# Optimization experiments

Hardware: AMD Instinct MI355X
Metric: run time of the kernel (lower is better)

The kernel has to match this reference:

```python
import jax, jax.numpy as jnp
import numpy as np

N_NODES = 50000
N_EDGES = 800000
N_GRAPHS = 64
HEADS = 4
IN_CH, HID_CH, OUT_CH = 128, 64, 32


def setup_inputs() -> dict:
    key = jax.random.key(0)
    ks = jax.random.split(key, 13)
    x = jax.random.normal(ks[0], (N_NODES, IN_CH), dtype=jnp.float32)
    edge_index = jax.random.randint(ks[1], (2, N_EDGES), 0, N_NODES, dtype=jnp.int64)
    tensor_batch = jnp.sort(jax.random.randint(ks[2], (N_NODES,), 0, N_GRAPHS, dtype=jnp.int64))
    s = 0.1
    return {
        "x": x,
        "edge_index": edge_index,
        "tensor_batch": tensor_batch,
        "W1": jax.random.normal(ks[3], (IN_CH, HEADS * HID_CH), dtype=jnp.float32) * s,
        "a_src1": jax.random.normal(ks[4], (HEADS, HID_CH), dtype=jnp.float32) * s,
        "a_dst1": jax.random.normal(ks[5], (HEADS, HID_CH), dtype=jnp.float32) * s,
        "b1": jnp.zeros((HEADS * HID_CH,), dtype=jnp.float32),
        "W2": jax.random.normal(ks[6], (HEADS * HID_CH, HEADS * OUT_CH), dtype=jnp.float32) * s,
        "a_src2": jax.random.normal(ks[7], (HEADS, OUT_CH), dtype=jnp.float32) * s,
        "a_dst2": jax.random.normal(ks[8], (HEADS, OUT_CH), dtype=jnp.float32) * s,
        "b2": jnp.zeros((HEADS * OUT_CH,), dtype=jnp.float32),
        "Wout": jax.random.normal(ks[9], (HEADS * OUT_CH, 2), dtype=jnp.float32) * s,
        "bout": jnp.zeros((2,), dtype=jnp.float32),
    }


def gat_conv(x, src, dst, W, a_src, a_dst, b, heads, ch):
    """PyG-style GATConv (eval mode, self-loops already appended)."""
    N = x.shape[0]
    h = (x @ W).reshape(N, heads, ch)            # [N,H,C] per-head projection
    s = jnp.sum(h * a_src, axis=-1)              # [N,H] source attention term
    d = jnp.sum(h * a_dst, axis=-1)              # [N,H] dest attention term
    e = jax.nn.leaky_relu(s[src] + d[dst], negative_slope=0.2)   # [E,H]
    # segment softmax over incoming edges of each destination node
    m = jax.ops.segment_max(e, dst, num_segments=N)              # [N,H]
    ex = jnp.exp(e - m[dst])
    denom = jax.ops.segment_sum(ex, dst, num_segments=N)         # [N,H]
    alpha = ex / (denom[dst] + 1e-16)                            # [E,H]
    out = jax.ops.segment_sum(h[src] * alpha[:, :, None], dst, num_segments=N)
    return out.reshape(N, heads * ch) + b


def reference(x, edge_index, tensor_batch, W1, a_src1, a_dst1, b1,
              W2, a_src2, a_dst2, b2, Wout, bout):
    N = x.shape[0]
    loop = jnp.arange(N, dtype=edge_index.dtype)
    src = jnp.concatenate([edge_index[0], loop])  # add self-loops (PyG default)
    dst = jnp.concatenate([edge_index[1], loop])
    h = jax.nn.relu(gat_conv(x, src, dst, W1, a_src1, a_dst1, b1, HEADS, HID_CH))
    h = jax.nn.relu(gat_conv(h, src, dst, W2, a_src2, a_dst2, b2, HEADS, OUT_CH))
    # global mean pool per graph
    sums = jax.ops.segment_sum(h, tensor_batch, num_segments=N_GRAPHS)
    counts = jax.ops.segment_sum(jnp.ones((N, 1), h.dtype), tensor_batch, num_segments=N_GRAPHS)
    pooled = sums / jnp.maximum(counts, 1.0)
    logits = pooled @ Wout + bout
    return jax.nn.softmax(logits, axis=-1)
```

## Files before the change

kernel.cpp:

```cpp
#include <hip/hip_runtime.h>
#include <hip/hip_bf16.h>

#define N_NODES 50000
#define N_EDGES 800000
#define N_GRAPHS 64
#define HEADS 4
#define IN_CH 128
#define HID 64
#define F1 256
#define OUT_CH 32
#define F2 128
#define POOL_SPLITS 16
#define SCAN_B 256
#define SCAN_NB ((N_NODES + SCAN_B - 1) / SCAN_B)
#define GEMM_GRID ((N_NODES + 127) / 128)
#define COUNT_GRID ((N_EDGES + 255) / 256)
#define XPACK_GRID (N_NODES * IN_CH / 8 / 256)

typedef unsigned short ushortT;
typedef unsigned int uintT;
typedef short v8s __attribute__((ext_vector_type(8)));
typedef float v4f __attribute__((ext_vector_type(4)));
typedef float v2f __attribute__((ext_vector_type(2)));

__device__ __forceinline__ ushortT f2bf(float f) {
    union { float f; unsigned int i; } v; v.f = f;
    unsigned int x = v.i;
    unsigned int r = (x + 0x7fffu + ((x >> 16) & 1u)) >> 16;
    return (ushortT)r;
}
__device__ __forceinline__ float bf_lo(uintT w) {
    union { unsigned int i; float f; } v; v.i = w << 16; return v.f;
}
__device__ __forceinline__ float bf_hi(uintT w) {
    union { unsigned int i; float f; } v; v.i = w & 0xffff0000u; return v.f;
}
__device__ __forceinline__ unsigned char f2fp8(float f) {
    return (unsigned char)__builtin_amdgcn_cvt_pk_fp8_f32(f, f, 0u, false);
}

__device__ __forceinline__ void packW_one(const float* __restrict__ W,
                                          uint4* __restrict__ dst,
                                          int i, int FIN, int FOUT) {
    int KC = FIN / 32;
    int lane = i & 63, g = i >> 6;
    int kc = g % KC, nt = g / KC;
    int n = nt * 16 + (lane & 15);
    int kbase = kc * 32 + (lane >> 4) * 8;
    union { uint4 q; ushortT u[8]; } pk;
#pragma unroll
    for (int j = 0; j < 8; j++) pk.u[j] = f2bf(W[(kbase + j) * FOUT + n]);
    dst[i] = pk.q;
}

__global__ __launch_bounds__(256) void k_pack(
        const float* __restrict__ x, const float* __restrict__ W1,
        const float* __restrict__ W2, uint4* __restrict__ wpk,
        ushortT* __restrict__ xb) {
    int b = blockIdx.x;
    if (b < 32) {
        int i = b * 256 + threadIdx.x;
        if (i < 4096) packW_one(W1, wpk, i, IN_CH, F1);
        else          packW_one(W2, wpk + 4096, i - 4096, F1, F2);
    } else {
        long i = (long)(b - 32) * 256 + threadIdx.x;
        const float4* xf = (const float4*)x + i * 2;
        float4 a = xf[0], c = xf[1];
        union { uint4 q; ushortT u[8]; } pk;
        pk.u[0] = f2bf(a.x); pk.u[1] = f2bf(a.y);
        pk.u[2] = f2bf(a.z); pk.u[3] = f2bf(a.w);
        pk.u[4] = f2bf(c.x); pk.u[5] = f2bf(c.y);
        pk.u[6] = f2bf(c.z); pk.u[7] = f2bf(c.w);
        ((uint4*)xb)[i] = pk.q;
    }
}

template <int FIN, int FOUT>
__device__ __forceinline__ void gemm_body(const ushortT* __restrict__ A,
                                          const uint4* __restrict__ Wpk,
                                          const float* __restrict__ ASrc,
                                          const float* __restrict__ ADst,
                                          unsigned char* __restrict__ out,
                                          float* __restrict__ s_out_g,
                                          float* __restrict__ d_out_g,
                                          int nrows, int bid) {
    constexpr int KC = FIN / 32;
    constexpr int NT = FOUT / 16;
    constexpr int NTH = (FOUT / HEADS) / 16;
    int tid = threadIdx.x;
    int wave = tid >> 6, lane = tid & 63;
    long rowA = (long)bid * 128 + wave * 32;
    long rowB = rowA + 16;
    bool doA = rowA < nrows, doB = rowB < nrows;
    if (!doA) return;
    int m = lane & 15, b = lane >> 4;

    v8s afA[KC], afB[KC];
#pragma unroll
    for (int kc = 0; kc < KC; kc++) {
        union { v8s v; uint4 q; } u;
        u.q = *(const uint4*)(A + (rowA + m) * FIN + kc * 32 + b * 8);
        afA[kc] = u.v;
        if (doB) {
            u.q = *(const uint4*)(A + (rowB + m) * FIN + kc * 32 + b * 8);
            afB[kc] = u.v;
        }
    }

    float spA[4] = {0,0,0,0}, dpA[4] = {0,0,0,0};
    float spB[4] = {0,0,0,0}, dpB[4] = {0,0,0,0};
    float skA[4], dkA[4], skB[4], dkB[4];
#pragma unroll
    for (int nt = 0; nt < NT; nt++) {
        v4f cA = {0.f, 0.f, 0.f, 0.f}, cB = {0.f, 0.f, 0.f, 0.f};
#pragma unroll
        for (int kc = 0; kc < KC; kc++) {
            union { v8s v; uint4 q; } bu;
            bu.q = Wpk[(nt * KC + kc) * 64 + lane];
            cA = __builtin_amdgcn_mfma_f32_16x16x32_bf16(afA[kc], bu.v, cA, 0, 0, 0);
            if (doB)
                cB = __builtin_amdgcn_mfma_f32_16x16x32_bf16(afB[kc], bu.v, cB, 0, 0, 0);
        }
        int col = nt * 16 + m;
        float av = ASrc[col], dv = ADst[col];
        long rA = rowA + b * 4;
#pragma unroll
        for (int reg = 0; reg < 4; reg++) {
            out[(rA + reg) * FOUT + col] = f2fp8(cA[reg]);
            spA[reg] += cA[reg] * av;
            dpA[reg] += cA[reg] * dv;
        }
        if (doB) {
            long rB = rowB + b * 4;
#pragma unroll
            for (int reg = 0; reg < 4; reg++) {
                out[(rB + reg) * FOUT + col] = f2fp8(cB[reg]);
                spB[reg] += cB[reg] * av;
                dpB[reg] += cB[reg] * dv;
            }
        }
        if ((nt % NTH) == NTH - 1) {
#pragma unroll
            for (int o = 1; o < 16; o <<= 1) {
#pragma unroll
                for (int reg = 0; reg < 4; reg++) {
                    spA[reg] += __shfl_xor(spA[reg], o, 64);
                    dpA[reg] += __shfl_xor(dpA[reg], o, 64);
                    spB[reg] += __shfl_xor(spB[reg], o, 64);
                    dpB[reg] += __shfl_xor(dpB[reg], o, 64);
                }
            }
            int hd = nt / NTH;
#pragma unroll
            for (int reg = 0; reg < 4; reg++) {
                if (m == hd) {
                    skA[reg] = spA[reg]; dkA[reg] = dpA[reg];
                    skB[reg] = spB[reg]; dkB[reg] = dpB[reg];
                }
                spA[reg] = 0.f; dpA[reg] = 0.f;
                spB[reg] = 0.f; dpB[reg] = 0.f;
            }
        }
    }
    if (m < HEADS) {
        long rA = rowA + b * 4;
#pragma unroll
        for (int reg = 0; reg < 4; reg++) {
            s_out_g[(rA + reg) * HEADS + m] = skA[reg];
            d_out_g[(rA + reg) * HEADS + m] = dkA[reg];
        }
        if (doB) {
            long rB = rowB + b * 4;
#pragma unroll
            for (int reg = 0; reg < 4; reg++) {
                s_out_g[(rB + reg) * HEADS + m] = skB[reg];
                d_out_g[(rB + reg) * HEADS + m] = dkB[reg];
            }
        }
    }
}

__global__ __launch_bounds__(256) void k_mega1(
        const ushortT* __restrict__ xb, const uint4* __restrict__ wpk,
        const float* __restrict__ asrc1, const float* __restrict__ adst1,
        unsigned char* __restrict__ u_h, float* __restrict__ f_s,
        float* __restrict__ f_d, const int* __restrict__ ei,
        int* __restrict__ counts, int* __restrict__ rank) {
    if (blockIdx.x < GEMM_GRID) {
        gemm_body<IN_CH, F1>(xb, wpk, asrc1, adst1, u_h, f_s, f_d,
                             N_NODES, blockIdx.x);
    } else {
        int e = (blockIdx.x - GEMM_GRID) * 256 + threadIdx.x;
        if (e < N_EDGES) {
            int dst = ei[N_EDGES + e];
            rank[e] = atomicAdd(&counts[dst], 1);
        }
    }
}

__global__ __launch_bounds__(256) void k_gemm2(
        const ushortT* __restrict__ A, const uint4* __restrict__ wpk2,
        const float* __restrict__ asrc2, const float* __restrict__ adst2,
        unsigned char* __restrict__ u_h, float* __restrict__ f_s,
        float* __restrict__ f_d) {
    gemm_body<F1, F2>(A, wpk2, asrc2, adst2, u_h, f_s, f_d,
                      N_NODES, blockIdx.x);
}

__global__ void k_scan1(const int* __restrict__ counts, int* __restrict__ offs,
                        int* __restrict__ bsum) {
    __shared__ int sh[SCAN_B];
    int b = blockIdx.x, t = threadIdx.x;
    int i = b * SCAN_B + t;
    int v = (i < N_NODES) ? counts[i] : 0;
    sh[t] = v;
    __syncthreads();
    for (int o = 1; o < SCAN_B; o <<= 1) {
        int add = (t >= o) ? sh[t - o] : 0;
        __syncthreads();
        sh[t] += add;
        __syncthreads();
    }
    if (i < N_NODES) offs[i] = sh[t] - v;
    if (t == SCAN_B - 1) bsum[b] = sh[t];
}

__global__ void k_scan2(const int* __restrict__ bsum, int* __restrict__ bbase,
                        int* __restrict__ offs, const int* __restrict__ batch,
                        int* __restrict__ bounds) {
    __shared__ int sh[SCAN_B];
    int t = threadIdx.x;
    int v = (t < SCAN_NB) ? bsum[t] : 0;
    sh[t] = v;
    __syncthreads();
    for (int o = 1; o < SCAN_B; o <<= 1) {
        int add = (t >= o) ? sh[t - o] : 0;
        __syncthreads();
        sh[t] += add;
        __syncthreads();
    }
    if (t < SCAN_NB) bbase[t] = sh[t] - v;
    if (t == SCAN_B - 1) offs[N_NODES] = sh[t];
    if (t <= N_GRAPHS) {
        int lo = 0, hi = N_NODES;
        while (lo < hi) {
            int mid = (lo + hi) >> 1;
            if (batch[mid] < t) lo = mid + 1; else hi = mid;
        }
        bounds[t] = lo;
    }
}

__global__ void k_scatter(const int* __restrict__ ei, const int* __restrict__ offs,
                          const int* __restrict__ bbase, const int* __restrict__ rank,
                          int* __restrict__ csr_src) {
    int e = blockIdx.x * blockDim.x + threadIdx.x;
    if (e >= N_EDGES) return;
    int src = ei[e], dst = ei[N_EDGES + e];
    int pos = offs[dst] + bbase[dst >> 8] + rank[e];
    csr_src[pos] = src;
}

template <int C, int VEC, int WPB, int CHUNK>
__global__ __launch_bounds__(64 * WPB) void k_agg(
        const unsigned char* __restrict__ hb, const float* __restrict__ s,
        const float* __restrict__ d, const int* __restrict__ offs,
        const int* __restrict__ bbase, const int* __restrict__ csr_src,
        const float* __restrict__ bias, ushortT* __restrict__ xout) {
    constexpr int F = HEADS * C;
    constexpr int TPN = F / VEC;
    static_assert(TPN == 32, "two nodes per wave");
    static_assert(C / VEC == 8, "head = tl>>3");
    static_assert(N_NODES % (WPB * 2) == 0, "exact grid");
    __shared__ int lsrc[WPB][2][CHUNK];
    __shared__ float lex[WPB][2][CHUNK * HEADS];
    int wv = threadIdx.x >> 6;
    int t = threadIdx.x & 63;
    int half = t >> 5, tl = t & 31;
    int n = (blockIdx.x * WPB + wv) * 2 + half;
    int h = tl >> 3;
    int beg = offs[n] + bbase[n >> 8];
    int np1 = n + 1;
    int end = (np1 < N_NODES) ? offs[np1] + bbase[np1 >> 8] : offs[N_NODES];
    float4 dn = *(const float4*)(d + n * 4);

    float4 svn = *(const float4*)(s + n * 4);
    float ssel = (h == 0) ? svn.x : (h == 1) ? svn.y : (h == 2) ? svn.z : svn.w;
    float dsel = (h == 0) ? dn.x : (h == 1) ? dn.y : (h == 2) ? dn.z : dn.w;
    float es = ssel + dsel; es = es > 0.f ? es : 0.2f * es;
    float exs = __expf(es);
    float sumex = exs;
    float acc[VEC];
    if (VEC == 8) {
        uint2 w = ((const uint2*)hb)[(long)n * TPN + tl];
        v2f p0 = __builtin_amdgcn_cvt_pk_f32_fp8(w.x, false);
        v2f p1 = __builtin_amdgcn_cvt_pk_f32_fp8(w.x, true);
        v2f p2 = __builtin_amdgcn_cvt_pk_f32_fp8(w.y, false);
        v2f p3 = __builtin_amdgcn_cvt_pk_f32_fp8(w.y, true);
        acc[0] = exs * p0.x; acc[1] = exs * p0.y;
        acc[2] = exs * p1.x; acc[3] = exs * p1.y;
        acc[4] = exs * p2.x; acc[5] = exs * p2.y;
        acc[6] = exs * p3.x; acc[7] = exs * p3.y;
    } else {
        uintT w = ((const uintT*)hb)[(long)n * TPN + tl];
        v2f p0 = __builtin_amdgcn_cvt_pk_f32_fp8(w, false);
        v2f p1 = __builtin_amdgcn_cvt_pk_f32_fp8(w, true);
        acc[0] = exs * p0.x; acc[1] = exs * p0.y;
        acc[2] = exs * p1.x; acc[3] = exs * p1.y;
    }

    int tot = end - beg;
    int totO = __shfl_xor(tot, 32, 64);
    int maxTot = max(tot, totO);
    for (int base = 0; base < maxTot; base += CHUNK) {
        int cnt = min(CHUNK, tot - base); if (cnt < 0) cnt = 0;
        int cntW = min(CHUNK, maxTot - base);
        for (int i = tl; i < cnt; i += TPN) {
            int sn = csr_src[beg + base + i];
            lsrc[wv][half][i] = sn;
            float4 sv = *(const float4*)(s + sn * 4);
            float e0 = sv.x + dn.x; e0 = e0 > 0.f ? e0 : 0.2f * e0;
            float e1 = sv.y + dn.y; e1 = e1 > 0.f ? e1 : 0.2f * e1;
            float e2 = sv.z + dn.z; e2 = e2 > 0.f ? e2 : 0.2f * e2;
            float e3 = sv.w + dn.w; e3 = e3 > 0.f ? e3 : 0.2f * e3;
            float4 exv = { __expf(e0), __expf(e1), __expf(e2), __expf(e3) };
            *(float4*)&lex[wv][half][i * 4] = exv;
        }
        asm volatile("s_waitcnt lgkmcnt(0)" ::: "memory");
#pragma unroll 4
        for (int i = 0; i < cntW; i++) {
            bool act = i < cnt;
            float ex = act ? lex[wv][half][i * 4 + h] : 0.f;
            int sn = act ? lsrc[wv][half][i] : 0;
            sumex += ex;
            if (VEC == 8) {
                uint2 w = ((const uint2*)hb)[(long)sn * TPN + tl];
                v2f p0 = __builtin_amdgcn_cvt_pk_f32_fp8(w.x, false);
                v2f p1 = __builtin_amdgcn_cvt_pk_f32_fp8(w.x, true);
                v2f p2 = __builtin_amdgcn_cvt_pk_f32_fp8(w.y, false);
                v2f p3 = __builtin_amdgcn_cvt_pk_f32_fp8(w.y, true);
                acc[0] += ex * p0.x; acc[1] += ex * p0.y;
                acc[2] += ex * p1.x; acc[3] += ex * p1.y;
                acc[4] += ex * p2.x; acc[5] += ex * p2.y;
                acc[6] += ex * p3.x; acc[7] += ex * p3.y;
            } else {
                uintT w = ((const uintT*)hb)[(long)sn * TPN + tl];
                v2f p0 = __builtin_amdgcn_cvt_pk_f32_fp8(w, false);
                v2f p1 = __builtin_amdgcn_cvt_pk_f32_fp8(w, true);
                acc[0] += ex * p0.x; acc[1] += ex * p0.y;
                acc[2] += ex * p1.x; acc[3] += ex * p1.y;
            }
        }
        asm volatile("" ::: "memory");
    }
    float inv = 1.f / (sumex + 1e-16f);
    float o[VEC];
#pragma unroll
    for (int j = 0; j < VEC; j++)
        o[j] = fmaxf(acc[j] * inv + bias[tl * VEC + j], 0.f);
    if (VEC == 8) {
        uint4 pk;
        pk.x = (uintT)f2bf(o[0]) | ((uintT)f2bf(o[1]) << 16);
        pk.y = (uintT)f2bf(o[2]) | ((uintT)f2bf(o[3]) << 16);
        pk.z = (uintT)f2bf(o[4]) | ((uintT)f2bf(o[5]) << 16);
        pk.w = (uintT)f2bf(o[6]) | ((uintT)f2bf(o[7]) << 16);
        ((uint4*)xout)[(long)n * TPN + tl] = pk;
    } else {
        uint2 pk;
        pk.x = (uintT)f2bf(o[0]) | ((uintT)f2bf(o[1]) << 16);
        pk.y = (uintT)f2bf(o[2]) | ((uintT)f2bf(o[3]) << 16);
        ((uint2*)xout)[(long)n * TPN + tl] = pk;
    }
}

__global__ void k_pool_partial(const ushortT* __restrict__ x2, const int* __restrict__ bounds,
                               float* __restrict__ partial) {
    int g = blockIdx.x, s = blockIdx.y;
    int t = threadIdx.x;
    int n0 = bounds[g], n1 = bounds[g + 1];
    int len = n1 - n0;
    int a = n0 + (int)((long)len * s / POOL_SPLITS);
    int b = n0 + (int)((long)len * (s + 1) / POOL_SPLITS);
    float acc = 0.f;
    for (int n = a; n < b; n++) acc += bf_lo((uintT)x2[(long)n * F2 + t]);
    partial[((long)g * POOL_SPLITS + s) * F2 + t] = acc;
}

__global__ void k_head(const float* __restrict__ partial, const int* __restrict__ bounds,
                       const float* __restrict__ Wout, const float* __restrict__ bout,
                       float* __restrict__ out) {
    __shared__ float red0[F2], red1[F2];
    int g = blockIdx.x;
    int t = threadIdx.x;
    int cntN = bounds[g + 1] - bounds[g];
    float cnt = fmaxf((float)cntN, 1.0f);
    float sum = 0.f;
    for (int s = 0; s < POOL_SPLITS; s++)
        sum += partial[((long)g * POOL_SPLITS + s) * F2 + t];
    float p = sum / cnt;
    red0[t] = p * Wout[t * 2 + 0];
    red1[t] = p * Wout[t * 2 + 1];
    __syncthreads();
    for (int off = F2 / 2; off > 0; off >>= 1) {
        if (t < off) { red0[t] += red0[t + off]; red1[t] += red1[t + off]; }
        __syncthreads();
    }
    if (t == 0) {
        float l0 = red0[0] + bout[0];
        float l1 = red1[0] + bout[1];
        float m = fmaxf(l0, l1);
        float e0 = __expf(l0 - m), e1 = __expf(l1 - m);
        float inv = 1.f / (e0 + e1);
        out[g * 2 + 0] = e0 * inv;
        out[g * 2 + 1] = e1 * inv;
    }
}

extern "C" void kernel_launch(void* const* d_in, const int* in_sizes, int n_in,
                              void* d_out, int out_size, void* d_ws, size_t ws_size,
                              hipStream_t stream) {
    const float* x     = (const float*)d_in[0];
    const int*   ei    = (const int*)d_in[1];
    const int*   batch = (const int*)d_in[2];
    const float* W1    = (const float*)d_in[3];
    const float* asrc1 = (const float*)d_in[4];
    const float* adst1 = (const float*)d_in[5];
    const float* b1    = (const float*)d_in[6];
    const float* W2    = (const float*)d_in[7];
    const float* asrc2 = (const float*)d_in[8];
    const float* adst2 = (const float*)d_in[9];
    const float* b2    = (const float*)d_in[10];
    const float* Wout  = (const float*)d_in[11];
    const float* bout  = (const float*)d_in[12];

    char* ws = (char*)d_ws;
    size_t off = 0;
    auto alloc = [&](size_t bytes) -> void* {
        void* p = ws + off;
        off += (bytes + 255) / 256 * 256;
        return p;
    };
    unsigned char* u_h = (unsigned char*)alloc((size_t)N_NODES * F1);
    ushortT* u_x1  = (ushortT*)alloc(sizeof(ushortT) * (size_t)N_NODES * F1);
    ushortT* u_x2  = (ushortT*)alloc(sizeof(ushortT) * (size_t)N_NODES * F2);
    ushortT* xb    = (ushortT*)alloc(sizeof(ushortT) * (size_t)N_NODES * IN_CH);
    uint4*   wpk   = (uint4*)alloc(sizeof(uint4) * 8192);
    float*   f_s   = (float*)alloc(sizeof(float) * (size_t)N_NODES * HEADS);
    float*   f_d   = (float*)alloc(sizeof(float) * (size_t)N_NODES * HEADS);
    int*     i_cnt = (int*)alloc(sizeof(int) * (size_t)N_NODES);
    int*     i_off = (int*)alloc(sizeof(int) * (size_t)(N_NODES + 1));
    int*     i_rnk = (int*)alloc(sizeof(int) * (size_t)N_EDGES);
    int*     i_csr = (int*)alloc(sizeof(int) * (size_t)N_EDGES);
    int*     i_bnd = (int*)alloc(sizeof(int) * (size_t)(N_GRAPHS + 1));
    int*     i_bs  = (int*)alloc(sizeof(int) * SCAN_NB);
    int*     i_bb  = (int*)alloc(sizeof(int) * SCAN_NB);
    float*   f_prt = (float*)alloc(sizeof(float) * (size_t)N_GRAPHS * POOL_SPLITS * F2);
    (void)ws_size; (void)in_sizes; (void)n_in; (void)out_size;

    hipMemsetAsync(i_cnt, 0, sizeof(int) * N_NODES, stream);

    k_pack<<<32 + XPACK_GRID, 256, 0, stream>>>(x, W1, W2, wpk, xb);

    k_mega1<<<GEMM_GRID + COUNT_GRID, 256, 0, stream>>>(
        xb, wpk, asrc1, adst1, u_h, f_s, f_d, ei, i_cnt, i_rnk);

    k_scan1<<<SCAN_NB, SCAN_B, 0, stream>>>(i_cnt, i_off, i_bs);
    k_scan2<<<1, SCAN_B, 0, stream>>>(i_bs, i_bb, i_off, batch, i_bnd);
    k_scatter<<<COUNT_GRID, 256, 0, stream>>>(ei, i_off, i_bb, i_rnk, i_csr);

    int agg_grid = N_NODES / (4 * 2);

    k_agg<HID, 8, 4, 128><<<agg_grid, 256, 0, stream>>>(
        u_h, f_s, f_d, i_off, i_bb, i_csr, b1, u_x1);

    k_gemm2<<<GEMM_GRID, 256, 0, stream>>>(u_x1, wpk + 4096, asrc2, adst2,
                                           u_h, f_s, f_d);
    k_agg<OUT_CH, 4, 4, 128><<<agg_grid, 256, 0, stream>>>(
        u_h, f_s, f_d, i_off, i_bb, i_csr, b2, u_x2);

    dim3 pgrid(N_GRAPHS, POOL_SPLITS);
    k_pool_partial<<<pgrid, F2, 0, stream>>>(u_x2, i_bnd, f_prt);
    k_head<<<N_GRAPHS, F2, 0, stream>>>(f_prt, i_bnd, Wout, bout, (float*)d_out);
}
```

Baseline: 270.3 us.

## Split GEMM work by head across waves with 16-row blocks

Restructures the fused projection GEMM so each block handles 16 rows and each of its four waves computes one attention head's column tiles, in place of each wave computing all columns for 32 rows. This raises the number of blocks and shortens each wave's serial MFMA chain, and the per-head score reduction becomes a single shuffle reduction with no head selection logic. In exchange, each block reloads the same A rows in all four waves, so A is fetched four times per block. The bounds check is dropped, which relies on N_NODES being divisible by 16.

Result: slower. 277.4 us (+2.6%).

```diff
diff --git a/kernel.cpp b/kernel.cpp
--- a/kernel.cpp
+++ b/kernel.cpp
@@ -13,7 +13,7 @@
 #define POOL_SPLITS 16
 #define SCAN_B 256
 #define SCAN_NB ((N_NODES + SCAN_B - 1) / SCAN_B)
-#define GEMM_GRID ((N_NODES + 127) / 128)
+#define GEMM_GRID (N_NODES / 16)
 #define COUNT_GRID ((N_EDGES + 255) / 256)
 #define XPACK_GRID (N_NODES * IN_CH / 8 / 256)
 
@@ -83,99 +83,55 @@
                                           unsigned char* __restrict__ out,
                                           float* __restrict__ s_out_g,
                                           float* __restrict__ d_out_g,
-                                          int nrows, int bid) {
+                                          int bid) {
     constexpr int KC = FIN / 32;
-    constexpr int NT = FOUT / 16;
     constexpr int NTH = (FOUT / HEADS) / 16;
     int tid = threadIdx.x;
     int wave = tid >> 6, lane = tid & 63;
-    long rowA = (long)bid * 128 + wave * 32;
-    long rowB = rowA + 16;
-    bool doA = rowA < nrows, doB = rowB < nrows;
-    if (!doA) return;
+    long row0 = (long)bid * 16;
     int m = lane & 15, b = lane >> 4;
 
-    v8s afA[KC], afB[KC];
+    v8s af[KC];
 #pragma unroll
     for (int kc = 0; kc < KC; kc++) {
         union { v8s v; uint4 q; } u;
-        u.q = *(const uint4*)(A + (rowA + m) * FIN + kc * 32 + b * 8);
-        afA[kc] = u.v;
-        if (doB) {
-            u.q = *(const uint4*)(A + (rowB + m) * FIN + kc * 32 + b * 8);
-            afB[kc] = u.v;
-        }
-    }
-
-    float spA[4] = {0,0,0,0}, dpA[4] = {0,0,0,0};
-    float spB[4] = {0,0,0,0}, dpB[4] = {0,0,0,0};
-    float skA[4], dkA[4], skB[4], dkB[4];
-#pragma unroll
-    for (int nt = 0; nt < NT; nt++) {
-        v4f cA = {0.f, 0.f, 0.f, 0.f}, cB = {0.f, 0.f, 0.f, 0.f};
+        u.q = *(const uint4*)(A + (row0 + m) * FIN + kc * 32 + b * 8);
+        af[kc] = u.v;
+    }
+
+    float sp[4] = {0,0,0,0}, dp[4] = {0,0,0,0};
+#pragma unroll
+    for (int j = 0; j < NTH; j++) {
+        int nt = wave * NTH + j;
+        v4f c = {0.f, 0.f, 0.f, 0.f};
 #pragma unroll
         for (int kc = 0; kc < KC; kc++) {
             union { v8s v; uint4 q; } bu;
             bu.q = Wpk[(nt * KC + kc) * 64 + lane];
-            cA = __builtin_amdgcn_mfma_f32_16x16x32_bf16(afA[kc], bu.v, cA, 0, 0, 0);
-            if (doB)
-                cB = __builtin_amdgcn_mfma_f32_16x16x32_bf16(afB[kc], bu.v, cB, 0, 0, 0);
+            c = __builtin_amdgcn_mfma_f32_16x16x32_bf16(af[kc], bu.v, c, 0, 0, 0);
         }
         int col = nt * 16 + m;
         float av = ASrc[col], dv = ADst[col];
-        long rA = rowA + b * 4;
 #pragma unroll
         for (int reg = 0; reg < 4; reg++) {
-            out[(rA + reg) * FOUT + col] = f2fp8(cA[reg]);
-            spA[reg] += cA[reg] * av;
-            dpA[reg] += cA[reg] * dv;
-        }
-        if (doB) {
-            long rB = rowB + b * 4;
-#pragma unroll
-            for (int reg = 0; reg < 4; reg++) {
-                out[(rB + reg) * FOUT + col] = f2fp8(cB[reg]);
-                spB[reg] += cB[reg] * av;
-                dpB[reg] += cB[reg] * dv;
-            }
-        }
-        if ((nt % NTH) == NTH - 1) {
-#pragma unroll
-            for (int o = 1; o < 16; o <<= 1) {
-#pragma unroll
-                for (int reg = 0; reg < 4; reg++) {
-                    spA[reg] += __shfl_xor(spA[reg], o, 64);
-                    dpA[reg] += __shfl_xor(dpA[reg], o, 64);
-                    spB[reg] += __shfl_xor(spB[reg], o, 64);
-                    dpB[reg] += __shfl_xor(dpB[reg], o, 64);
-                }
-            }
-            int hd = nt / NTH;
-#pragma unroll
-            for (int reg = 0; reg < 4; reg++) {
-                if (m == hd) {
-                    skA[reg] = spA[reg]; dkA[reg] = dpA[reg];
-                    skB[reg] = spB[reg]; dkB[reg] = dpB[reg];
-                }
-                spA[reg] = 0.f; dpA[reg] = 0.f;
-                spB[reg] = 0.f; dpB[reg] = 0.f;
-            }
-        }
-    }
-    if (m < HEADS) {
-        long rA = rowA + b * 4;
+            out[(row0 + b * 4 + reg) * FOUT + col] = f2fp8(c[reg]);
+            sp[reg] += c[reg] * av;
+            dp[reg] += c[reg] * dv;
+        }
+    }
+#pragma unroll
+    for (int o = 1; o < 16; o <<= 1) {
 #pragma unroll
         for (int reg = 0; reg < 4; reg++) {
-            s_out_g[(rA + reg) * HEADS + m] = skA[reg];
-            d_out_g[(rA + reg) * HEADS + m] = dkA[reg];
-        }
-        if (doB) {
-            long rB = rowB + b * 4;
-#pragma unroll
-            for (int reg = 0; reg < 4; reg++) {
-                s_out_g[(rB + reg) * HEADS + m] = skB[reg];
-                d_out_g[(rB + reg) * HEADS + m] = dkB[reg];
-            }
+            sp[reg] += __shfl_xor(sp[reg], o, 64);
+            dp[reg] += __shfl_xor(dp[reg], o, 64);
+        }
+    }
+    if (m == 0) {
+#pragma unroll
+        for (int reg = 0; reg < 4; reg++) {
+            s_out_g[(row0 + b * 4 + reg) * HEADS + wave] = sp[reg];
+            d_out_g[(row0 + b * 4 + reg) * HEADS + wave] = dp[reg];
         }
     }
 }
@@ -187,8 +143,7 @@
         float* __restrict__ f_d, const int* __restrict__ ei,
         int* __restrict__ counts, int* __restrict__ rank) {
     if (blockIdx.x < GEMM_GRID) {
-        gemm_body<IN_CH, F1>(xb, wpk, asrc1, adst1, u_h, f_s, f_d,
-                             N_NODES, blockIdx.x);
+        gemm_body<IN_CH, F1>(xb, wpk, asrc1, adst1, u_h, f_s, f_d, blockIdx.x);
     } else {
         int e = (blockIdx.x - GEMM_GRID) * 256 + threadIdx.x;
         if (e < N_EDGES) {
@@ -203,8 +158,7 @@
         const float* __restrict__ asrc2, const float* __restrict__ adst2,
         unsigned char* __restrict__ u_h, float* __restrict__ f_s,
         float* __restrict__ f_d) {
-    gemm_body<F1, F2>(A, wpk2, asrc2, adst2, u_h, f_s, f_d,
-                      N_NODES, blockIdx.x);
+    gemm_body<F1, F2>(A, wpk2, asrc2, adst2, u_h, f_s, f_d, blockIdx.x);
 }
 
 __global__ void k_scan1(const int* __restrict__ counts, int* __restrict__ offs,
```
